# Kernel optimization log

Hardware: AMD Instinct MI355X
Metric: run time of the kernel (lower is better)

Reference implementation:

```python
import jax, jax.numpy as jnp
import numpy as np

N_NODES = 50000
N_EDGES = 800000
N_REL = 6
N_LAYERS = 8
D = 256
NUM_GRAPHS = 512


def setup_inputs() -> dict:
    key = jax.random.key(0)
    ks = jax.random.split(key, 24)
    s = lambda *sh: 1.0 / np.sqrt(sh[0])
    inp = {
        "x": jax.random.normal(ks[0], (N_NODES, 13), dtype=jnp.float32),
        "edge_index": jax.random.randint(ks[1], (2, N_EDGES), 0, N_NODES, dtype=jnp.int64),
        "edge_type": jax.random.randint(ks[2], (N_EDGES,), 0, N_REL, dtype=jnp.int64),
        "batch": jnp.sort(jax.random.randint(ks[3], (N_NODES,), 0, NUM_GRAPHS, dtype=jnp.int64)),
        "enc_W": jax.random.normal(ks[4], (13, D), dtype=jnp.float32) * s(13),
        "enc_b": jnp.zeros((D,), dtype=jnp.float32),
        "prelu_a": jnp.float32(0.25),
        "rel_W": jax.random.normal(ks[5], (N_LAYERS, N_REL, D, D), dtype=jnp.float32) * s(D),
        "root_W": jax.random.normal(ks[6], (N_LAYERS, D, D), dtype=jnp.float32) * s(D),
        "conv_b": jnp.zeros((N_LAYERS, D), dtype=jnp.float32),
        "gp_W1": jax.random.normal(ks[7], (D, D), dtype=jnp.float32) * s(D),
        "gp_b1": jnp.zeros((D,), dtype=jnp.float32),
        "gp_W2": jax.random.normal(ks[8], (D, D), dtype=jnp.float32) * s(D),
        "gp_b2": jnp.zeros((D,), dtype=jnp.float32),
        "fc_W1": jax.random.normal(ks[9], (D, 1024), dtype=jnp.float32) * s(D),
        "fc_b1": jnp.zeros((1024,), dtype=jnp.float32),
        "fc_W2": jax.random.normal(ks[10], (1024, 512), dtype=jnp.float32) * s(1024),
        "fc_b2": jnp.zeros((512,), dtype=jnp.float32),
        "out_W": jax.random.normal(ks[11], (512, 1), dtype=jnp.float32) * s(512),
        "out_b": jnp.zeros((1,), dtype=jnp.float32),
    }
    return inp


def reference(x, edge_index, edge_type, batch, enc_W, enc_b, prelu_a, rel_W, root_W,
              conv_b, gp_W1, gp_b1, gp_W2, gp_b2, fc_W1, fc_b1, fc_W2, fc_b2, out_W, out_b):
    src, dst = edge_index[0], edge_index[1]
    h = x @ enc_W + enc_b  # [N, D]
    for i in range(N_LAYERS):
        skip = h
        # per-relation transform for all nodes: [R, N, D]
        xW = jnp.einsum('nd,rde->rne', h, rel_W[i])
        msgs = xW[edge_type, src]  # [E, D] gather by (relation, source node)
        agg = jax.ops.segment_sum(msgs, dst, num_segments=N_NODES)
        h = agg + h @ root_W[i] + conv_b[i]
        h = h + skip
        h = jnp.where(h > 0, h, prelu_a * h)  # PReLU (shared scalar)
        norm = jnp.sqrt(jnp.sum(h * h, axis=1, keepdims=True))
        h = h / jnp.maximum(norm, 1e-12)  # F.normalize(p=2, dim=1)
    g = jax.nn.relu(h @ gp_W1 + gp_b1) @ gp_W2 + gp_b2
    pooled = jax.ops.segment_sum(g, batch, num_segments=NUM_GRAPHS)  # global_add_pool
    z = jax.nn.relu(pooled @ fc_W1 + fc_b1)  # dropout = identity at eval
    z = jax.nn.relu(z @ fc_W2 + fc_b2)
    return jax.nn.relu(z @ out_W + out_b)  # [NUM_GRAPHS, 1]
```

## Files before the change

### kernel.cpp

```cpp
#include <hip/hip_runtime.h>

#define N_NODES   50000
#define N_EDGES   800000
#define N_REL     6
#define N_LAYERS  8
#define DD        256
#define NUM_GRAPHS 512

#define NKEYS      (N_REL * N_NODES)
#define SCAN_T     256
#define SCAN_E     8
#define SCAN_CHUNK (SCAN_T * SCAN_E)
#define SCAN_NB    ((NKEYS + SCAN_CHUNK - 1) / SCAN_CHUNK)

typedef _Float16 h4 __attribute__((ext_vector_type(4)));
typedef _Float16 h8 __attribute__((ext_vector_type(8)));
typedef float    f4 __attribute__((ext_vector_type(4)));

__device__ __forceinline__ void atomAddF(float* p, float v) { unsafeAtomicAdd(p, v); }

__device__ __forceinline__ void load_lds16(const void* g, void* l) {
    __builtin_amdgcn_global_load_lds(
        (const __attribute__((address_space(1))) uint32_t*)g,
        (__attribute__((address_space(3))) uint32_t*)l, 16, 0, 0);
}

__global__ __launch_bounds__(256) void enc_kernel(const float* __restrict__ x,
                                                  const float* __restrict__ W,
                                                  const float* __restrict__ b,
                                                  _Float16* __restrict__ Hhi,
                                                  _Float16* __restrict__ Hlo) {
    int n = blockIdx.x;
    int d = threadIdx.x;
    float s = b[d];
#pragma unroll
    for (int k = 0; k < 13; ++k) s = fmaf(x[n * 13 + k], W[k * 256 + d], s);
    const _Float16 hi = (_Float16)s;
    Hhi[(size_t)n * DD + d] = hi;
    Hlo[(size_t)n * DD + d] = (_Float16)(s - (float)hi);
}

__global__ __launch_bounds__(256) void wsplit_rel_kernel(const float* __restrict__ relW,
                                                         const float* __restrict__ rootW,
                                                         _Float16* __restrict__ wthi,
                                                         _Float16* __restrict__ wtlo) {
    const size_t id = (size_t)blockIdx.x * 256 + threadIdx.x;
    if (id >= (size_t)N_LAYERS * 7 * 256 * 256) return;
    const int k = (int)(id & 255);
    const int n = (int)((id >> 8) & 255);
    const int g = (int)((id >> 16) % 7);
    const int L = (int)((id >> 16) / 7);
    float w = (g < 6)
        ? relW[(((size_t)L * 6 + g) * 256 + k) * 256 + n]
        : rootW[((size_t)L * 256 + k) * 256 + n];
    if (g == 6 && k == n) w += 1.0f;
    const _Float16 hi = (_Float16)w;
    const size_t o = ((size_t)L * 256 + n) * 1792 + (size_t)g * 256 + k;
    wthi[o] = hi;
    wtlo[o] = (_Float16)(w - (float)hi);
}

__global__ __launch_bounds__(256) void wsplit_tr_kernel(const float* __restrict__ W,
                                                        _Float16* __restrict__ whi,
                                                        _Float16* __restrict__ wlo) {
    const int id = blockIdx.x * 256 + threadIdx.x;
    const int k = id & 255, n = id >> 8;
    const float w = W[(size_t)k * 256 + n];
    const _Float16 hi = (_Float16)w;
    whi[(size_t)n * 256 + k] = hi;
    wlo[(size_t)n * 256 + k] = (_Float16)(w - (float)hi);
}

template <int MODE>
__global__ __launch_bounds__(256, 2) void gemm_lds(
    const _Float16* __restrict__ Ahi, const _Float16* __restrict__ Alo,
    const _Float16* __restrict__ Hhi, const _Float16* __restrict__ Hlo,
    const _Float16* __restrict__ Bhi, const _Float16* __restrict__ Blo,
    int ldb, int boff_agg, int boff_h, int K_agg, int K_tot,
    float* __restrict__ Cf, _Float16* __restrict__ Ohi, _Float16* __restrict__ Olo,
    const float* __restrict__ bias, const float* __restrict__ pa,
    float* __restrict__ ss4, int M) {
    __shared__ _Float16 smem[16384];
    const int lane = threadIdx.x & 63;
    const int wave = threadIdx.x >> 6;
    const int lm = lane & 15, lq = lane >> 4;
    const int wm = wave & 1, wn = wave >> 1;
    const int mb = blockIdx.x * 128;
    const int nb = blockIdx.y * 128;

    int uoff[2], aoff[2], boff[2];
    int arowg[2], browg[2], achk[2];
#pragma unroll
    for (int q = 0; q < 2; ++q) {
        const int u    = (q * 4 + wave) * 64 + lane;
        const int row  = u >> 2;
        const int slot = u & 3;
        const int c    = slot ^ ((row >> 1) & 3);
        uoff[q] = (q * 4 + wave) * 64;
        int rg = mb + row; if (rg >= M) rg = M - 1;
        arowg[q] = rg;
        browg[q] = nb + row;
        achk[q]  = c * 8;
        (void)aoff; (void)boff;
    }

    f4 acc[4][4];
#pragma unroll
    for (int i = 0; i < 4; ++i)
#pragma unroll
        for (int j = 0; j < 4; ++j) acc[i][j] = (f4){0.f, 0.f, 0.f, 0.f};

    for (int k0 = 0; k0 < K_tot; k0 += 32) {
        const _Float16 *pAh, *pAl;
        int acol, bcol;
        if (k0 < K_agg) {
            const size_t pb = (size_t)(k0 >> 8) * (size_t)N_NODES * DD;
            pAh = Ahi + pb; pAl = Alo + pb;
            acol = k0 & 255;
            bcol = boff_agg + k0;
        } else {
            pAh = Hhi; pAl = Hlo;
            acol = k0 - K_agg;
            bcol = boff_h + (k0 - K_agg);
        }

        __syncthreads();
#pragma unroll
        for (int q = 0; q < 2; ++q) {
            const size_t ga = (size_t)arowg[q] * DD + acol + achk[q];
            const size_t gb = (size_t)browg[q] * ldb + bcol + achk[q];
            _Float16* lbase = smem + (size_t)uoff[q] * 8;
            load_lds16(pAh + ga, lbase);
            load_lds16(pAl + ga, lbase + 4096);
            load_lds16(Bhi + gb, lbase + 8192);
            load_lds16(Blo + gb, lbase + 12288);
        }
        __syncthreads();

        h8 ah[4], al[4], bh[4], bl[4];
#pragma unroll
        for (int i = 0; i < 4; ++i) {
            const int row  = wm * 64 + i * 16 + lm;
            const int slot = lq ^ ((row >> 1) & 3);
            const int o    = (row * 4 + slot) * 8;
            ah[i] = *(const h8*)(smem + o);
            al[i] = *(const h8*)(smem + 4096 + o);
        }
#pragma unroll
        for (int j = 0; j < 4; ++j) {
            const int n    = wn * 64 + j * 16 + lm;
            const int slot = lq ^ ((n >> 1) & 3);
            const int o    = (n * 4 + slot) * 8;
            bh[j] = *(const h8*)(smem + 8192 + o);
            bl[j] = *(const h8*)(smem + 12288 + o);
        }
#pragma unroll
        for (int i = 0; i < 4; ++i)
#pragma unroll
            for (int j = 0; j < 4; ++j) {
                acc[i][j] = __builtin_amdgcn_mfma_f32_16x16x32_f16(ah[i], bh[j], acc[i][j], 0, 0, 0);
                acc[i][j] = __builtin_amdgcn_mfma_f32_16x16x32_f16(ah[i], bl[j], acc[i][j], 0, 0, 0);
                acc[i][j] = __builtin_amdgcn_mfma_f32_16x16x32_f16(al[i], bh[j], acc[i][j], 0, 0, 0);
            }
    }

    if (MODE == 0) {
#pragma unroll
        for (int i = 0; i < 4; ++i)
#pragma unroll
            for (int r = 0; r < 4; ++r) {
                const int row = mb + wm * 64 + i * 16 + lq * 4 + r;
                if (row >= M) continue;
#pragma unroll
                for (int j = 0; j < 4; ++j) {
                    const int col = nb + wn * 64 + j * 16 + lm;
                    Cf[(size_t)row * DD + col] = acc[i][j][r] + bias[col];
                }
            }
    } else if (MODE == 3) {
#pragma unroll
        for (int i = 0; i < 4; ++i)
#pragma unroll
            for (int r = 0; r < 4; ++r) {
                const int row = mb + wm * 64 + i * 16 + lq * 4 + r;
                if (row >= M) continue;
#pragma unroll
                for (int j = 0; j < 4; ++j) {
                    const int col = nb + wn * 64 + j * 16 + lm;
                    Cf[(size_t)row * DD + col] += acc[i][j][r];
                }
            }
    } else if (MODE == 2) {
#pragma unroll
        for (int i = 0; i < 4; ++i)
#pragma unroll
            for (int r = 0; r < 4; ++r) {
                const int row = mb + wm * 64 + i * 16 + lq * 4 + r;
                if (row >= M) continue;
#pragma unroll
                for (int j = 0; j < 4; ++j) {
                    const int col = nb + wn * 64 + j * 16 + lm;
                    const float v = fmaxf(acc[i][j][r] + bias[col], 0.f);
                    const _Float16 hi = (_Float16)v;
                    const size_t idx = (size_t)row * DD + col;
                    Ohi[idx] = hi;
                    Olo[idx] = (_Float16)(v - (float)hi);
                }
            }
    } else {
        const float a = pa[0];
#pragma unroll
        for (int i = 0; i < 4; ++i)
#pragma unroll
            for (int r = 0; r < 4; ++r) {
                const int row = mb + wm * 64 + i * 16 + lq * 4 + r;
                float rss = 0.f;
                if (row < M) {
#pragma unroll
                    for (int j = 0; j < 4; ++j) {
                        const int col = nb + wn * 64 + j * 16 + lm;
                        float v = acc[i][j][r] + Cf[(size_t)row * DD + col];
                        v = v > 0.f ? v : a * v;
                        const _Float16 hi = (_Float16)v;
                        const size_t idx = (size_t)row * DD + col;
                        Ohi[idx] = hi;
                        Olo[idx] = (_Float16)(v - (float)hi);
                        rss = fmaf(v, v, rss);
                    }
                }
                rss += __shfl_xor(rss, 1, 64);
                rss += __shfl_xor(rss, 2, 64);
                rss += __shfl_xor(rss, 4, 64);
                rss += __shfl_xor(rss, 8, 64);
                if (lm == 0 && row < M)
                    ss4[(size_t)row * 4 + blockIdx.y * 2 + wn] = rss;
            }
    }
}

__global__ __launch_bounds__(256) void norm_kernel(_Float16* __restrict__ Hhi,
                                                   _Float16* __restrict__ Hlo,
                                                   const float* __restrict__ ss4) {
    const int node = blockIdx.x * 4 + (threadIdx.x >> 6);
    const int lane = threadIdx.x & 63;
    if (node >= N_NODES) return;
    const float tot = ss4[node * 4 + 0] + ss4[node * 4 + 1] +
                      ss4[node * 4 + 2] + ss4[node * 4 + 3];
    const float inv = 1.0f / fmaxf(sqrtf(tot), 1e-12f);
    const size_t o = (size_t)node * DD + lane * 4;
    h4 vh = *(const h4*)(Hhi + o);
    h4 vl = *(const h4*)(Hlo + o);
    h4 oh, ol;
#pragma unroll
    for (int e = 0; e < 4; ++e) {
        const float v = ((float)vh[e] + (float)vl[e]) * inv;
        oh[e] = (_Float16)v;
        ol[e] = (_Float16)(v - (float)oh[e]);
    }
    *(h4*)(Hhi + o) = oh;
    *(h4*)(Hlo + o) = ol;
}

__global__ __launch_bounds__(256) void hist_kernel(const int* __restrict__ dst,
                                                   const int* __restrict__ etype,
                                                   int* __restrict__ cnt) {
    const int e = blockIdx.x * 256 + threadIdx.x;
    if (e >= N_EDGES) return;
    atomicAdd(&cnt[etype[e] * N_NODES + dst[e]], 1);
}

__global__ __launch_bounds__(SCAN_T) void scan1_kernel(const int* __restrict__ cnt,
                                                       int* __restrict__ off,
                                                       int* __restrict__ bsum) {
    __shared__ int sh[SCAN_T];
    const int b = blockIdx.x, t = threadIdx.x;
    const int base = b * SCAN_CHUNK + t * SCAN_E;
    int pre[SCAN_E];
    int s = 0;
#pragma unroll
    for (int i = 0; i < SCAN_E; ++i) {
        const int x = (base + i < NKEYS) ? cnt[base + i] : 0;
        pre[i] = s;
        s += x;
    }
    sh[t] = s;
    __syncthreads();
    for (int d = 1; d < SCAN_T; d <<= 1) {
        const int x = (t >= d) ? sh[t - d] : 0;
        __syncthreads();
        sh[t] += x;
        __syncthreads();
    }
    const int toff = (t == 0) ? 0 : sh[t - 1];
#pragma unroll
    for (int i = 0; i < SCAN_E; ++i)
        if (base + i < NKEYS) off[base + i] = toff + pre[i];
    if (t == SCAN_T - 1) bsum[b] = sh[SCAN_T - 1];
}

__global__ __launch_bounds__(SCAN_T) void scan2_kernel(int* __restrict__ bsum, int n) {
    __shared__ int sh[SCAN_T];
    const int t = threadIdx.x;
    const int base = t * SCAN_E;
    int pre[SCAN_E];
    int s = 0;
#pragma unroll
    for (int i = 0; i < SCAN_E; ++i) {
        const int x = (base + i < n) ? bsum[base + i] : 0;
        pre[i] = s;
        s += x;
    }
    sh[t] = s;
    __syncthreads();
    for (int d = 1; d < SCAN_T; d <<= 1) {
        const int x = (t >= d) ? sh[t - d] : 0;
        __syncthreads();
        sh[t] += x;
        __syncthreads();
    }
    const int toff = (t == 0) ? 0 : sh[t - 1];
#pragma unroll
    for (int i = 0; i < SCAN_E; ++i)
        if (base + i < n) bsum[base + i] = toff + pre[i];
}

__global__ __launch_bounds__(SCAN_T) void scan3_kernel(int* __restrict__ off,
                                                       const int* __restrict__ bsum) {
    const int b = blockIdx.x, t = threadIdx.x;
    const int add = bsum[b];
    const int base = b * SCAN_CHUNK + t * SCAN_E;
#pragma unroll
    for (int i = 0; i < SCAN_E; ++i)
        if (base + i < NKEYS) off[base + i] += add;
    if (b == 0 && t == 0) off[NKEYS] = N_EDGES;
}

__global__ __launch_bounds__(256) void csr_fill_kernel(const int* __restrict__ src,
                                                       const int* __restrict__ dst,
                                                       const int* __restrict__ etype,
                                                       int* __restrict__ cursor,
                                                       int* __restrict__ sorted_src) {
    const int e = blockIdx.x * 256 + threadIdx.x;
    if (e >= N_EDGES) return;
    const int key = etype[e] * N_NODES + dst[e];
    const int pos = atomicAdd(&cursor[key], 1);
    sorted_src[pos] = src[e];
}

__global__ __launch_bounds__(256) void agg2_kernel(const _Float16* __restrict__ Hhi,
                                                   const _Float16* __restrict__ Hlo,
                                                   const int* __restrict__ off,
                                                   const int* __restrict__ isrc,
                                                   _Float16* __restrict__ agghi,
                                                   _Float16* __restrict__ agglo, int rel0) {
    const int node = blockIdx.x * 4 + (threadIdx.x >> 6);
    const int lane = threadIdx.x & 63;
    if (node >= N_NODES) return;
#pragma unroll
    for (int rl = 0; rl < 2; ++rl) {
        const int r = rel0 + rl;
        const int s0 = off[r * N_NODES + node];
        const int s1 = off[r * N_NODES + node + 1];
        float a0 = 0.f, a1 = 0.f, a2 = 0.f, a3 = 0.f;
        for (int e = s0; e < s1; ++e) {
            const int s = isrc[e];
            const h4 vh = *(const h4*)(Hhi + (size_t)s * DD + lane * 4);
            const h4 vl = *(const h4*)(Hlo + (size_t)s * DD + lane * 4);
            a0 += (float)vh[0] + (float)vl[0];
            a1 += (float)vh[1] + (float)vl[1];
            a2 += (float)vh[2] + (float)vl[2];
            a3 += (float)vh[3] + (float)vl[3];
        }
        h4 oh, ol;
        oh[0] = (_Float16)a0; ol[0] = (_Float16)(a0 - (float)oh[0]);
        oh[1] = (_Float16)a1; ol[1] = (_Float16)(a1 - (float)oh[1]);
        oh[2] = (_Float16)a2; ol[2] = (_Float16)(a2 - (float)oh[2]);
        oh[3] = (_Float16)a3; ol[3] = (_Float16)(a3 - (float)oh[3]);
        const size_t o = ((size_t)rl * N_NODES + node) * DD + lane * 4;
        *(h4*)(agghi + o) = oh;
        *(h4*)(agglo + o) = ol;
    }
}

__global__ __launch_bounds__(256) void gemm128x64(const float* __restrict__ A,
                                                  const float* __restrict__ B,
                                                  float* __restrict__ C,
                                                  const float* __restrict__ bias,
                                                  int M, int N, int K) {
    __shared__ float As[16 * 132];
    __shared__ float Bs[16 * 68];
    const int t  = threadIdx.x;
    const int tx = t & 15;
    const int ty = t >> 4;
    const int m0 = blockIdx.x * 128;
    const int n0 = blockIdx.y * 64;
    const int arow = t >> 2;
    const int ak   = (t & 3) * 4;
    const int bk   = t >> 4;
    const int bc   = (t & 15) * 4;

    float acc[8][4];
#pragma unroll
    for (int i = 0; i < 8; ++i)
#pragma unroll
        for (int j = 0; j < 4; ++j) acc[i][j] = 0.f;

    for (int k0 = 0; k0 < K; k0 += 16) {
        float4 a0 = {0.f, 0.f, 0.f, 0.f}, a1 = {0.f, 0.f, 0.f, 0.f};
        const int r0 = m0 + arow, r1 = r0 + 64;
        if (r0 < M) a0 = *reinterpret_cast<const float4*>(A + (size_t)r0 * K + k0 + ak);
        if (r1 < M) a1 = *reinterpret_cast<const float4*>(A + (size_t)r1 * K + k0 + ak);
        const float4 bb = *reinterpret_cast<const float4*>(B + (size_t)(k0 + bk) * N + n0 + bc);
        __syncthreads();
        As[(ak + 0) * 132 + arow] = a0.x;
        As[(ak + 1) * 132 + arow] = a0.y;
        As[(ak + 2) * 132 + arow] = a0.z;
        As[(ak + 3) * 132 + arow] = a0.w;
        As[(ak + 0) * 132 + arow + 64] = a1.x;
        As[(ak + 1) * 132 + arow + 64] = a1.y;
        As[(ak + 2) * 132 + arow + 64] = a1.z;
        As[(ak + 3) * 132 + arow + 64] = a1.w;
        *reinterpret_cast<float4*>(&Bs[bk * 68 + bc]) = bb;
        __syncthreads();
#pragma unroll
        for (int k = 0; k < 16; ++k) {
            const float4 fa0 = *reinterpret_cast<const float4*>(&As[k * 132 + ty * 8]);
            const float4 fa1 = *reinterpret_cast<const float4*>(&As[k * 132 + ty * 8 + 4]);
            const float4 fb  = *reinterpret_cast<const float4*>(&Bs[k * 68 + tx * 4]);
            const float av[8] = {fa0.x, fa0.y, fa0.z, fa0.w, fa1.x, fa1.y, fa1.z, fa1.w};
            const float bv[4] = {fb.x, fb.y, fb.z, fb.w};
#pragma unroll
            for (int i = 0; i < 8; ++i)
#pragma unroll
                for (int j = 0; j < 4; ++j) acc[i][j] = fmaf(av[i], bv[j], acc[i][j]);
        }
    }
    const int row = m0 + ty * 8;
    const int col = n0 + tx * 4;
    const float4 bv = *reinterpret_cast<const float4*>(bias + col);
#pragma unroll
    for (int i = 0; i < 8; ++i) {
        const int m = row + i;
        if (m >= M) continue;
        float4 v = {acc[i][0], acc[i][1], acc[i][2], acc[i][3]};
        v.x = fmaxf(v.x + bv.x, 0.f); v.y = fmaxf(v.y + bv.y, 0.f);
        v.z = fmaxf(v.z + bv.z, 0.f); v.w = fmaxf(v.w + bv.w, 0.f);
        *reinterpret_cast<float4*>(C + (size_t)m * N + col) = v;
    }
}

__global__ __launch_bounds__(64) void pool_kernel(const float* __restrict__ g,
                                                  const int* __restrict__ batch,
                                                  float* __restrict__ pooled) {
    const int c     = threadIdx.x;
    const int start = blockIdx.x * 128;
    const int end   = min(start + 128, N_NODES);
    int cur = batch[start];
    float4 acc = {0.f, 0.f, 0.f, 0.f};
    for (int n = start; n < end; ++n) {
        const int bn = batch[n];
        if (bn != cur) {
            float* p = pooled + (size_t)cur * DD + c * 4;
            atomAddF(p + 0, acc.x); atomAddF(p + 1, acc.y);
            atomAddF(p + 2, acc.z); atomAddF(p + 3, acc.w);
            acc = {0.f, 0.f, 0.f, 0.f};
            cur = bn;
        }
        const float4 v = reinterpret_cast<const float4*>(g + (size_t)n * DD)[c];
        acc.x += v.x; acc.y += v.y; acc.z += v.z; acc.w += v.w;
    }
    float* p = pooled + (size_t)cur * DD + c * 4;
    atomAddF(p + 0, acc.x); atomAddF(p + 1, acc.y);
    atomAddF(p + 2, acc.z); atomAddF(p + 3, acc.w);
}

__global__ __launch_bounds__(64) void out_kernel(const float* __restrict__ z2,
                                                 const float* __restrict__ W,
                                                 const float* __restrict__ b,
                                                 float* __restrict__ out) {
    const int g = blockIdx.x;
    const int t = threadIdx.x;
    float s = 0.f;
#pragma unroll
    for (int j = 0; j < 8; ++j) s = fmaf(z2[(size_t)g * 512 + t + 64 * j], W[t + 64 * j], s);
#pragma unroll
    for (int off = 32; off; off >>= 1) s += __shfl_xor(s, off, 64);
    if (t == 0) {
        const float v = s + b[0];
        out[g] = v > 0.f ? v : 0.f;
    }
}

extern "C" void kernel_launch(void* const* d_in, const int* in_sizes, int n_in,
                              void* d_out, int out_size, void* d_ws, size_t ws_size,
                              hipStream_t stream) {
    const float* x       = (const float*)d_in[0];
    const int*   eidx    = (const int*)d_in[1];
    const int*   etype   = (const int*)d_in[2];
    const int*   batch   = (const int*)d_in[3];
    const float* enc_W   = (const float*)d_in[4];
    const float* enc_b   = (const float*)d_in[5];
    const float* prelu_a = (const float*)d_in[6];
    const float* rel_W   = (const float*)d_in[7];
    const float* root_W  = (const float*)d_in[8];
    const float* conv_b  = (const float*)d_in[9];
    const float* gp_W1   = (const float*)d_in[10];
    const float* gp_b1   = (const float*)d_in[11];
    const float* gp_W2   = (const float*)d_in[12];
    const float* gp_b2   = (const float*)d_in[13];
    const float* fc_W1   = (const float*)d_in[14];
    const float* fc_b1   = (const float*)d_in[15];
    const float* fc_W2   = (const float*)d_in[16];
    const float* fc_b2   = (const float*)d_in[17];
    const float* out_W   = (const float*)d_in[18];
    const float* out_b   = (const float*)d_in[19];
    float* out = (float*)d_out;

    uint8_t* wp = (uint8_t*)d_ws;
    auto alloc = [&](size_t bytes) {
        void* r = (void*)wp;
        wp += (bytes + 255) & ~(size_t)255;
        return r;
    };
    float*    base   = (float*)alloc((size_t)N_NODES * DD * 4);
    _Float16* Hhi    = (_Float16*)alloc((size_t)N_NODES * DD * 2);
    _Float16* Hlo    = (_Float16*)alloc((size_t)N_NODES * DD * 2);
    _Float16* agghi  = (_Float16*)alloc((size_t)2 * N_NODES * DD * 2);
    _Float16* agglo  = (_Float16*)alloc((size_t)2 * N_NODES * DD * 2);
    _Float16* wthi   = (_Float16*)alloc((size_t)N_LAYERS * 256 * 1792 * 2);
    _Float16* wtlo   = (_Float16*)alloc((size_t)N_LAYERS * 256 * 1792 * 2);
    _Float16* wtg1hi = (_Float16*)alloc((size_t)256 * 256 * 2);
    _Float16* wtg1lo = (_Float16*)alloc((size_t)256 * 256 * 2);
    _Float16* wtg2hi = (_Float16*)alloc((size_t)256 * 256 * 2);
    _Float16* wtg2lo = (_Float16*)alloc((size_t)256 * 256 * 2);
    float*    ss4    = (float*)alloc((size_t)N_NODES * 4 * 4);
    float*    pooled = (float*)alloc((size_t)NUM_GRAPHS * DD * 4);
    float*    z1     = (float*)alloc((size_t)NUM_GRAPHS * 1024 * 4);
    float*    z2     = (float*)alloc((size_t)NUM_GRAPHS * 512 * 4);
    int*      ioff   = (int*)alloc((size_t)(NKEYS + 1) * 4);
    int*      icur   = (int*)alloc((size_t)NKEYS * 4);
    int*      ibsum  = (int*)alloc(256 * 4);
    int*      isrc   = (int*)alloc((size_t)N_EDGES * 4);

    const int* src = eidx;
    const int* dst = eidx + N_EDGES;

    const size_t wtot = (size_t)N_LAYERS * 7 * 256 * 256;
    wsplit_rel_kernel<<<(int)((wtot + 255) / 256), 256, 0, stream>>>(rel_W, root_W, wthi, wtlo);
    wsplit_tr_kernel<<<256, 256, 0, stream>>>(gp_W1, wtg1hi, wtg1lo);
    wsplit_tr_kernel<<<256, 256, 0, stream>>>(gp_W2, wtg2hi, wtg2lo);

    hipMemsetAsync(icur, 0, (size_t)NKEYS * sizeof(int), stream);
    const int eb = (N_EDGES + 255) / 256;
    hist_kernel<<<eb, 256, 0, stream>>>(dst, etype, icur);
    scan1_kernel<<<SCAN_NB, SCAN_T, 0, stream>>>(icur, ioff, ibsum);
    scan2_kernel<<<1, SCAN_T, 0, stream>>>(ibsum, SCAN_NB);
    scan3_kernel<<<SCAN_NB, SCAN_T, 0, stream>>>(ioff, ibsum);
    hipMemcpyAsync(icur, ioff, (size_t)NKEYS * sizeof(int), hipMemcpyDeviceToDevice, stream);
    csr_fill_kernel<<<eb, 256, 0, stream>>>(src, dst, etype, icur, isrc);

    enc_kernel<<<N_NODES, 256, 0, stream>>>(x, enc_W, enc_b, Hhi, Hlo);

    const dim3 gG((N_NODES + 127) / 128, 2);
    const int  nodeb = (N_NODES + 3) / 4;

    for (int L = 0; L < N_LAYERS; ++L) {
        const _Float16* Bh = wthi + (size_t)L * 256 * 1792;
        const _Float16* Bl = wtlo + (size_t)L * 256 * 1792;
        agg2_kernel<<<nodeb, 256, 0, stream>>>(Hhi, Hlo, ioff, isrc, agghi, agglo, 0);
        gemm_lds<0><<<gG, 256, 0, stream>>>(agghi, agglo, Hhi, Hlo, Bh, Bl,
                                            1792, 0, 1536, 512, 768,
                                            base, nullptr, nullptr,
                                            conv_b + L * DD, nullptr, nullptr, N_NODES);
        agg2_kernel<<<nodeb, 256, 0, stream>>>(Hhi, Hlo, ioff, isrc, agghi, agglo, 2);
        gemm_lds<3><<<gG, 256, 0, stream>>>(agghi, agglo, Hhi, Hlo, Bh, Bl,
                                            1792, 512, 0, 512, 512,
                                            base, nullptr, nullptr,
                                            nullptr, nullptr, nullptr, N_NODES);
        agg2_kernel<<<nodeb, 256, 0, stream>>>(Hhi, Hlo, ioff, isrc, agghi, agglo, 4);
        gemm_lds<1><<<gG, 256, 0, stream>>>(agghi, agglo, Hhi, Hlo, Bh, Bl,
                                            1792, 1024, 0, 512, 512,
                                            base, Hhi, Hlo,
                                            nullptr, prelu_a, ss4, N_NODES);
        norm_kernel<<<nodeb, 256, 0, stream>>>(Hhi, Hlo, ss4);
    }

    gemm_lds<2><<<gG, 256, 0, stream>>>(nullptr, nullptr, Hhi, Hlo, wtg1hi, wtg1lo,
                                        256, 0, 0, 0, 256,
                                        nullptr, agghi, agglo, gp_b1, nullptr, nullptr, N_NODES);
    gemm_lds<0><<<gG, 256, 0, stream>>>(agghi, agglo, nullptr, nullptr, wtg2hi, wtg2lo,
                                        256, 0, 0, 256, 256,
                                        base, nullptr, nullptr, gp_b2, nullptr, nullptr, N_NODES);

    hipMemsetAsync(pooled, 0, (size_t)NUM_GRAPHS * DD * sizeof(float), stream);
    pool_kernel<<<(N_NODES + 127) / 128, 64, 0, stream>>>(base, batch, pooled);

    gemm128x64<<<dim3(4, 16), 256, 0, stream>>>(pooled, fc_W1, z1, fc_b1,
                                                NUM_GRAPHS, 1024, DD);
    gemm128x64<<<dim3(4, 8), 256, 0, stream>>>(z1, fc_W2, z2, fc_b2,
                                               NUM_GRAPHS, 512, 1024);
    out_kernel<<<NUM_GRAPHS, 64, 0, stream>>>(z2, out_W, out_b, out);
}
```

Before: 3.702 ms.

## Run FC head GEMMs on split-fp16 MFMA path and flatten aggregation grid

The two small FP32 SIMT GEMMs in the MLP head are replaced with the split-fp16 MFMA gemm_lds kernel. To support this, the kernel gains lda/ldc strides, the FC weights are pre-split and transposed, and the pooled output is split into hi/lo halves. The aggregation kernel now assigns one wave per (relation, node) pair instead of looping over two relations per wave, which doubles the grid and is meant to improve load balance. Extra split kernels and launches are added, and the split-fp16 scheme may differ numerically from plain FP32.

```diff
diff --git a/kernel.cpp b/kernel.cpp
--- a/kernel.cpp
+++ b/kernel.cpp
@@ -62,13 +62,26 @@
 
 __global__ __launch_bounds__(256) void wsplit_tr_kernel(const float* __restrict__ W,
                                                         _Float16* __restrict__ whi,
-                                                        _Float16* __restrict__ wlo) {
+                                                        _Float16* __restrict__ wlo,
+                                                        int K, int N) {
+    const size_t id = (size_t)blockIdx.x * 256 + threadIdx.x;
+    if (id >= (size_t)K * N) return;
+    const int k = (int)(id % K), n = (int)(id / K);
+    const float w = W[(size_t)k * N + n];
+    const _Float16 hi = (_Float16)w;
+    whi[(size_t)n * K + k] = hi;
+    wlo[(size_t)n * K + k] = (_Float16)(w - (float)hi);
+}
+
+__global__ __launch_bounds__(256) void fsplit_kernel(const float* __restrict__ S,
+                                                     _Float16* __restrict__ hi,
+                                                     _Float16* __restrict__ lo, int total) {
     const int id = blockIdx.x * 256 + threadIdx.x;
-    const int k = id & 255, n = id >> 8;
-    const float w = W[(size_t)k * 256 + n];
-    const _Float16 hi = (_Float16)w;
-    whi[(size_t)n * 256 + k] = hi;
-    wlo[(size_t)n * 256 + k] = (_Float16)(w - (float)hi);
+    if (id >= total) return;
+    const float v = S[id];
+    const _Float16 h = (_Float16)v;
+    hi[id] = h;
+    lo[id] = (_Float16)(v - (float)h);
 }
 
 template <int MODE>
@@ -76,7 +89,7 @@
     const _Float16* __restrict__ Ahi, const _Float16* __restrict__ Alo,
     const _Float16* __restrict__ Hhi, const _Float16* __restrict__ Hlo,
     const _Float16* __restrict__ Bhi, const _Float16* __restrict__ Blo,
-    int ldb, int boff_agg, int boff_h, int K_agg, int K_tot,
+    int lda, int ldb, int ldc, int boff_agg, int boff_h, int K_agg, int K_tot,
     float* __restrict__ Cf, _Float16* __restrict__ Ohi, _Float16* __restrict__ Olo,
     const float* __restrict__ bias, const float* __restrict__ pa,
     float* __restrict__ ss4, int M) {
@@ -88,8 +101,7 @@
     const int mb = blockIdx.x * 128;
     const int nb = blockIdx.y * 128;
 
-    int uoff[2], aoff[2], boff[2];
-    int arowg[2], browg[2], achk[2];
+    int uoff[2], arowg[2], browg[2], achk[2];
 #pragma unroll
     for (int q = 0; q < 2; ++q) {
         const int u    = (q * 4 + wave) * 64 + lane;
@@ -101,7 +113,6 @@
         arowg[q] = rg;
         browg[q] = nb + row;
         achk[q]  = c * 8;
-        (void)aoff; (void)boff;
     }
 
     f4 acc[4][4];
@@ -127,7 +138,7 @@
         __syncthreads();
 #pragma unroll
         for (int q = 0; q < 2; ++q) {
-            const size_t ga = (size_t)arowg[q] * DD + acol + achk[q];
+            const size_t ga = (size_t)arowg[q] * lda + acol + achk[q];
             const size_t gb = (size_t)browg[q] * ldb + bcol + achk[q];
             _Float16* lbase = smem + (size_t)uoff[q] * 8;
             load_lds16(pAh + ga, lbase);
@@ -174,7 +185,7 @@
 #pragma unroll
                 for (int j = 0; j < 4; ++j) {
                     const int col = nb + wn * 64 + j * 16 + lm;
-                    Cf[(size_t)row * DD + col] = acc[i][j][r] + bias[col];
+                    Cf[(size_t)row * ldc + col] = acc[i][j][r] + bias[col];
                 }
             }
     } else if (MODE == 3) {
@@ -187,7 +198,7 @@
 #pragma unroll
                 for (int j = 0; j < 4; ++j) {
                     const int col = nb + wn * 64 + j * 16 + lm;
-                    Cf[(size_t)row * DD + col] += acc[i][j][r];
+                    Cf[(size_t)row * ldc + col] += acc[i][j][r];
                 }
             }
     } else if (MODE == 2) {
@@ -202,7 +213,7 @@
                     const int col = nb + wn * 64 + j * 16 + lm;
                     const float v = fmaxf(acc[i][j][r] + bias[col], 0.f);
                     const _Float16 hi = (_Float16)v;
-                    const size_t idx = (size_t)row * DD + col;
+                    const size_t idx = (size_t)row * ldc + col;
                     Ohi[idx] = hi;
                     Olo[idx] = (_Float16)(v - (float)hi);
                 }
@@ -219,10 +230,10 @@
 #pragma unroll
                     for (int j = 0; j < 4; ++j) {
                         const int col = nb + wn * 64 + j * 16 + lm;
-                        float v = acc[i][j][r] + Cf[(size_t)row * DD + col];
+                        float v = acc[i][j][r] + Cf[(size_t)row * ldc + col];
                         v = v > 0.f ? v : a * v;
                         const _Float16 hi = (_Float16)v;
-                        const size_t idx = (size_t)row * DD + col;
+                        const size_t idx = (size_t)row * ldc + col;
                         Ohi[idx] = hi;
                         Olo[idx] = (_Float16)(v - (float)hi);
                         rss = fmaf(v, v, rss);
@@ -353,100 +364,32 @@
                                                    const int* __restrict__ isrc,
                                                    _Float16* __restrict__ agghi,
                                                    _Float16* __restrict__ agglo, int rel0) {
-    const int node = blockIdx.x * 4 + (threadIdx.x >> 6);
+    const int pair = blockIdx.x * 4 + (threadIdx.x >> 6);
     const int lane = threadIdx.x & 63;
-    if (node >= N_NODES) return;
-#pragma unroll
-    for (int rl = 0; rl < 2; ++rl) {
-        const int r = rel0 + rl;
-        const int s0 = off[r * N_NODES + node];
-        const int s1 = off[r * N_NODES + node + 1];
-        float a0 = 0.f, a1 = 0.f, a2 = 0.f, a3 = 0.f;
-        for (int e = s0; e < s1; ++e) {
-            const int s = isrc[e];
-            const h4 vh = *(const h4*)(Hhi + (size_t)s * DD + lane * 4);
-            const h4 vl = *(const h4*)(Hlo + (size_t)s * DD + lane * 4);
-            a0 += (float)vh[0] + (float)vl[0];
-            a1 += (float)vh[1] + (float)vl[1];
-            a2 += (float)vh[2] + (float)vl[2];
-            a3 += (float)vh[3] + (float)vl[3];
-        }
-        h4 oh, ol;
-        oh[0] = (_Float16)a0; ol[0] = (_Float16)(a0 - (float)oh[0]);
-        oh[1] = (_Float16)a1; ol[1] = (_Float16)(a1 - (float)oh[1]);
-        oh[2] = (_Float16)a2; ol[2] = (_Float16)(a2 - (float)oh[2]);
-        oh[3] = (_Float16)a3; ol[3] = (_Float16)(a3 - (float)oh[3]);
-        const size_t o = ((size_t)rl * N_NODES + node) * DD + lane * 4;
-        *(h4*)(agghi + o) = oh;
-        *(h4*)(agglo + o) = ol;
-    }
-}
-
-__global__ __launch_bounds__(256) void gemm128x64(const float* __restrict__ A,
-                                                  const float* __restrict__ B,
-                                                  float* __restrict__ C,
-                                                  const float* __restrict__ bias,
-                                                  int M, int N, int K) {
-    __shared__ float As[16 * 132];
-    __shared__ float Bs[16 * 68];
-    const int t  = threadIdx.x;
-    const int tx = t & 15;
-    const int ty = t >> 4;
-    const int m0 = blockIdx.x * 128;
-    const int n0 = blockIdx.y * 64;
-    const int arow = t >> 2;
-    const int ak   = (t & 3) * 4;
-    const int bk   = t >> 4;
-    const int bc   = (t & 15) * 4;
-
-    float acc[8][4];
-#pragma unroll
-    for (int i = 0; i < 8; ++i)
-#pragma unroll
-        for (int j = 0; j < 4; ++j) acc[i][j] = 0.f;
-
-    for (int k0 = 0; k0 < K; k0 += 16) {
-        float4 a0 = {0.f, 0.f, 0.f, 0.f}, a1 = {0.f, 0.f, 0.f, 0.f};
-        const int r0 = m0 + arow, r1 = r0 + 64;
-        if (r0 < M) a0 = *reinterpret_cast<const float4*>(A + (size_t)r0 * K + k0 + ak);
-        if (r1 < M) a1 = *reinterpret_cast<const float4*>(A + (size_t)r1 * K + k0 + ak);
-        const float4 bb = *reinterpret_cast<const float4*>(B + (size_t)(k0 + bk) * N + n0 + bc);
-        __syncthreads();
-        As[(ak + 0) * 132 + arow] = a0.x;
-        As[(ak + 1) * 132 + arow] = a0.y;
-        As[(ak + 2) * 132 + arow] = a0.z;
-        As[(ak + 3) * 132 + arow] = a0.w;
-        As[(ak + 0) * 132 + arow + 64] = a1.x;
-        As[(ak + 1) * 132 + arow + 64] = a1.y;
-        As[(ak + 2) * 132 + arow + 64] = a1.z;
-        As[(ak + 3) * 132 + arow + 64] = a1.w;
-        *reinterpret_cast<float4*>(&Bs[bk * 68 + bc]) = bb;
-        __syncthreads();
-#pragma unroll
-        for (int k = 0; k < 16; ++k) {
-            const float4 fa0 = *reinterpret_cast<const float4*>(&As[k * 132 + ty * 8]);
-            const float4 fa1 = *reinterpret_cast<const float4*>(&As[k * 132 + ty * 8 + 4]);
-            const float4 fb  = *reinterpret_cast<const float4*>(&Bs[k * 68 + tx * 4]);
-            const float av[8] = {fa0.x, fa0.y, fa0.z, fa0.w, fa1.x, fa1.y, fa1.z, fa1.w};
-            const float bv[4] = {fb.x, fb.y, fb.z, fb.w};
-#pragma unroll
-            for (int i = 0; i < 8; ++i)
-#pragma unroll
-                for (int j = 0; j < 4; ++j) acc[i][j] = fmaf(av[i], bv[j], acc[i][j]);
-        }
-    }
-    const int row = m0 + ty * 8;
-    const int col = n0 + tx * 4;
-    const float4 bv = *reinterpret_cast<const float4*>(bias + col);
-#pragma unroll
-    for (int i = 0; i < 8; ++i) {
-        const int m = row + i;
-        if (m >= M) continue;
-        float4 v = {acc[i][0], acc[i][1], acc[i][2], acc[i][3]};
-        v.x = fmaxf(v.x + bv.x, 0.f); v.y = fmaxf(v.y + bv.y, 0.f);
-        v.z = fmaxf(v.z + bv.z, 0.f); v.w = fmaxf(v.w + bv.w, 0.f);
-        *reinterpret_cast<float4*>(C + (size_t)m * N + col) = v;
-    }
+    if (pair >= 2 * N_NODES) return;
+    const int rl   = (pair >= N_NODES) ? 1 : 0;
+    const int node = pair - rl * N_NODES;
+    const int r    = rel0 + rl;
+    const int s0 = off[r * N_NODES + node];
+    const int s1 = off[r * N_NODES + node + 1];
+    float a0 = 0.f, a1 = 0.f, a2 = 0.f, a3 = 0.f;
+    for (int e = s0; e < s1; ++e) {
+        const int s = isrc[e];
+        const h4 vh = *(const h4*)(Hhi + (size_t)s * DD + lane * 4);
+        const h4 vl = *(const h4*)(Hlo + (size_t)s * DD + lane * 4);
+        a0 += (float)vh[0] + (float)vl[0];
+        a1 += (float)vh[1] + (float)vl[1];
+        a2 += (float)vh[2] + (float)vl[2];
+        a3 += (float)vh[3] + (float)vl[3];
+    }
+    h4 oh, ol;
+    oh[0] = (_Float16)a0; ol[0] = (_Float16)(a0 - (float)oh[0]);
+    oh[1] = (_Float16)a1; ol[1] = (_Float16)(a1 - (float)oh[1]);
+    oh[2] = (_Float16)a2; ol[2] = (_Float16)(a2 - (float)oh[2]);
+    oh[3] = (_Float16)a3; ol[3] = (_Float16)(a3 - (float)oh[3]);
+    const size_t o = ((size_t)rl * N_NODES + node) * DD + lane * 4;
+    *(h4*)(agghi + o) = oh;
+    *(h4*)(agglo + o) = ol;
 }
 
 __global__ __launch_bounds__(64) void pool_kernel(const float* __restrict__ g,
@@ -474,7 +417,8 @@
     atomAddF(p + 2, acc.z); atomAddF(p + 3, acc.w);
 }
 
-__global__ __launch_bounds__(64) void out_kernel(const float* __restrict__ z2,
+__global__ __launch_bounds__(64) void out_kernel(const _Float16* __restrict__ z2hi,
+                                                 const _Float16* __restrict__ z2lo,
                                                  const float* __restrict__ W,
                                                  const float* __restrict__ b,
                                                  float* __restrict__ out) {
@@ -482,7 +426,11 @@
     const int t = threadIdx.x;
     float s = 0.f;
 #pragma unroll
-    for (int j = 0; j < 8; ++j) s = fmaf(z2[(size_t)g * 512 + t + 64 * j], W[t + 64 * j], s);
+    for (int j = 0; j < 8; ++j) {
+        const int idx = t + 64 * j;
+        const float z = (float)z2hi[(size_t)g * 512 + idx] + (float)z2lo[(size_t)g * 512 + idx];
+        s = fmaf(z, W[idx], s);
+    }
 #pragma unroll
     for (int off = 32; off; off >>= 1) s += __shfl_xor(s, off, 64);
     if (t == 0) {
@@ -533,10 +481,18 @@
     _Float16* wtg1lo = (_Float16*)alloc((size_t)256 * 256 * 2);
     _Float16* wtg2hi = (_Float16*)alloc((size_t)256 * 256 * 2);
     _Float16* wtg2lo = (_Float16*)alloc((size_t)256 * 256 * 2);
+    _Float16* wtf1hi = (_Float16*)alloc((size_t)1024 * 256 * 2);
+    _Float16* wtf1lo = (_Float16*)alloc((size_t)1024 * 256 * 2);
+    _Float16* wtf2hi = (_Float16*)alloc((size_t)512 * 1024 * 2);
+    _Float16* wtf2lo = (_Float16*)alloc((size_t)512 * 1024 * 2);
     float*    ss4    = (float*)alloc((size_t)N_NODES * 4 * 4);
     float*    pooled = (float*)alloc((size_t)NUM_GRAPHS * DD * 4);
-    float*    z1     = (float*)alloc((size_t)NUM_GRAPHS * 1024 * 4);
-    float*    z2     = (float*)alloc((size_t)NUM_GRAPHS * 512 * 4);
+    _Float16* phi    = (_Float16*)alloc((size_t)NUM_GRAPHS * DD * 2);
+    _Float16* plo    = (_Float16*)alloc((size_t)NUM_GRAPHS * DD * 2);
+    _Float16* z1hi   = (_Float16*)alloc((size_t)NUM_GRAPHS * 1024 * 2);
+    _Float16* z1lo   = (_Float16*)alloc((size_t)NUM_GRAPHS * 1024 * 2);
+    _Float16* z2hi   = (_Float16*)alloc((size_t)NUM_GRAPHS * 512 * 2);
+    _Float16* z2lo   = (_Float16*)alloc((size_t)NUM_GRAPHS * 512 * 2);
     int*      ioff   = (int*)alloc((size_t)(NKEYS + 1) * 4);
     int*      icur   = (int*)alloc((size_t)NKEYS * 4);
     int*      ibsum  = (int*)alloc(256 * 4);
@@ -547,8 +503,10 @@
 
     const size_t wtot = (size_t)N_LAYERS * 7 * 256 * 256;
     wsplit_rel_kernel<<<(int)((wtot + 255) / 256), 256, 0, stream>>>(rel_W, root_W, wthi, wtlo);
-    wsplit_tr_kernel<<<256, 256, 0, stream>>>(gp_W1, wtg1hi, wtg1lo);
-    wsplit_tr_kernel<<<256, 256, 0, stream>>>(gp_W2, wtg2hi, wtg2lo);
+    wsplit_tr_kernel<<<256, 256, 0, stream>>>(gp_W1, wtg1hi, wtg1lo, 256, 256);
+    wsplit_tr_kernel<<<256, 256, 0, stream>>>(gp_W2, wtg2hi, wtg2lo, 256, 256);
+    wsplit_tr_kernel<<<1024, 256, 0, stream>>>(fc_W1, wtf1hi, wtf1lo, 256, 1024);
+    wsplit_tr_kernel<<<2048, 256, 0, stream>>>(fc_W2, wtf2hi, wtf2lo, 1024, 512);
 
     hipMemsetAsync(icur, 0, (size_t)NKEYS * sizeof(int), stream);
     const int eb = (N_EDGES + 255) / 256;
@@ -563,41 +521,48 @@
 
     const dim3 gG((N_NODES + 127) / 128, 2);
     const int  nodeb = (N_NODES + 3) / 4;
+    const int  aggb  = (2 * N_NODES + 3) / 4;
 
     for (int L = 0; L < N_LAYERS; ++L) {
         const _Float16* Bh = wthi + (size_t)L * 256 * 1792;
         const _Float16* Bl = wtlo + (size_t)L * 256 * 1792;
-        agg2_kernel<<<nodeb, 256, 0, stream>>>(Hhi, Hlo, ioff, isrc, agghi, agglo, 0);
+        agg2_kernel<<<aggb, 256, 0, stream>>>(Hhi, Hlo, ioff, isrc, agghi, agglo, 0);
         gemm_lds<0><<<gG, 256, 0, stream>>>(agghi, agglo, Hhi, Hlo, Bh, Bl,
-                                            1792, 0, 1536, 512, 768,
+                                            256, 1792, 256, 0, 1536, 512, 768,
                                             base, nullptr, nullptr,
                                             conv_b + L * DD, nullptr, nullptr, N_NODES);
-        agg2_kernel<<<nodeb, 256, 0, stream>>>(Hhi, Hlo, ioff, isrc, agghi, agglo, 2);
+        agg2_kernel<<<aggb, 256, 0, stream>>>(Hhi, Hlo, ioff, isrc, agghi, agglo, 2);
         gemm_lds<3><<<gG, 256, 0, stream>>>(agghi, agglo, Hhi, Hlo, Bh, Bl,
-                                            1792, 512, 0, 512, 512,
+                                            256, 1792, 256, 512, 0, 512, 512,
                                             base, nullptr, nullptr,
                                             nullptr, nullptr, nullptr, N_NODES);
-        agg2_kernel<<<nodeb, 256, 0, stream>>>(Hhi, Hlo, ioff, isrc, agghi, agglo, 4);
+        agg2_kernel<<<aggb, 256, 0, stream>>>(Hhi, Hlo, ioff, isrc, agghi, agglo, 4);
         gemm_lds<1><<<gG, 256, 0, stream>>>(agghi, agglo, Hhi, Hlo, Bh, Bl,
-                                            1792, 1024, 0, 512, 512,
+                                            256, 1792, 256, 1024, 0, 512, 512,
                                             base, Hhi, Hlo,
                                             nullptr, prelu_a, ss4, N_NODES);
         norm_kernel<<<nodeb, 256, 0, stream>>>(Hhi, Hlo, ss4);
     }
 
     gemm_lds<2><<<gG, 256, 0, stream>>>(nullptr, nullptr, Hhi, Hlo, wtg1hi, wtg1lo,
-                                        256, 0, 0, 0, 256,
+                                        256, 256, 256, 0, 0, 0, 256,
                                         nullptr, agghi, agglo, gp_b1, nullptr, nullptr, N_NODES);
     gemm_lds<0><<<gG, 256, 0, stream>>>(agghi, agglo, nullptr, nullptr, wtg2hi, wtg2lo,
-                                        256, 0, 0, 256, 256,
+                                        256, 256, 256, 0, 0, 256, 256,
                                         base, nullptr, nullptr, gp_b2, nullptr, nullptr, N_NODES);
 
     hipMemsetAsync(pooled, 0, (size_t)NUM_GRAPHS * DD * sizeof(float), stream);
     pool_kernel<<<(N_NODES + 127) / 128, 64, 0, stream>>>(base, batch, pooled);
-
-    gemm128x64<<<dim3(4, 16), 256, 0, stream>>>(pooled, fc_W1, z1, fc_b1,
-                                                NUM_GRAPHS, 1024, DD);
-    gemm128x64<<<dim3(4, 8), 256, 0, stream>>>(z1, fc_W2, z2, fc_b2,
-                                               NUM_GRAPHS, 512, 1024);
-    out_kernel<<<NUM_GRAPHS, 64, 0, stream>>>(z2, out_W, out_b, out);
-}
+    fsplit_kernel<<<(NUM_GRAPHS * DD + 255) / 256, 256, 0, stream>>>(
+        pooled, phi, plo, NUM_GRAPHS * DD);
+
+    gemm_lds<2><<<dim3(4, 8), 256, 0, stream>>>(nullptr, nullptr, phi, plo, wtf1hi, wtf1lo,
+                                                256, 256, 1024, 0, 0, 0, 256,
+                                                nullptr, z1hi, z1lo, fc_b1, nullptr, nullptr,
+                                                NUM_GRAPHS);
+    gemm_lds<2><<<dim3(4, 4), 256, 0, stream>>>(nullptr, nullptr, z1hi, z1lo, wtf2hi, wtf2lo,
+                                                1024, 1024, 512, 0, 0, 0, 1024,
+                                                nullptr, z2hi, z2lo, fc_b2, nullptr, nullptr,
+                                                NUM_GRAPHS);
+    out_kernel<<<NUM_GRAPHS, 64, 0, stream>>>(z2hi, z2lo, out_W, out_b, out);
+}
```

Result: no change. 3.633 ms (-1.9%).
